# Kernel optimization log

Measured on AMD Instinct MI355X. Metric: run time of the kernel, lower is better.

The kernel has to match this reference:

```python
import jax, jax.numpy as jnp
import numpy as np

NEG_INF = -1.0e9  # matches the -1e9 mask constant in the torch module


def setup_inputs() -> dict:
    key = jax.random.key(0)
    k1, k2, k3, k4, k5 = jax.random.split(key, 5)
    B, S, D = 8, 2048, 1024
    x = jax.random.normal(k1, (B, S, D), dtype=jnp.float32)
    mask = jax.random.randint(k2, (B, S), 0, 2, dtype=jnp.int32)
    # torch.nn.Linear stores weight as [out_features, in_features]
    scale = 1.0 / np.sqrt(D)
    w_q = jax.random.normal(k3, (D, D), dtype=jnp.float32) * scale
    w_k = jax.random.normal(k4, (D, D), dtype=jnp.float32) * scale
    w_v = jax.random.normal(k5, (D, D), dtype=jnp.float32) * scale
    return {"x": x, "mask": mask, "w_q": w_q, "w_k": w_k, "w_v": w_v}


def reference(x, mask, w_q, w_k, w_v):
    # Linear (no bias): y = x @ W^T
    q = jnp.einsum("bsd,ed->bse", x, w_q)
    k = jnp.einsum("bsd,ed->bse", x, w_k)
    v = jnp.einsum("bsd,ed->bse", x, w_v)
    # raw (unscaled) scores, exactly as in the torch module
    s = jnp.einsum("bqd,bkd->bqk", q, k)  # [B, S, S]
    # dropout p=0.0 -> identity (eval mode); mask added AFTER dropout
    s = s + NEG_INF * mask.astype(s.dtype)[:, None, :]  # broadcast over query dim
    s = jax.nn.softmax(s, axis=-1)
    out = jnp.einsum("bqk,bkd->bqd", s, v)
    return out, s
```

## Files before the change

### kernel.cpp

```cpp
#include <hip/hip_runtime.h>

#define NEG_INF_F (-1.0e9f)

typedef _Float16 f16x8 __attribute__((ext_vector_type(8)));
typedef float f32x4 __attribute__((ext_vector_type(4)));

__device__ inline unsigned short f16_of(float f) {
    _Float16 h = (_Float16)f;
    return __builtin_bit_cast(unsigned short, h);
}
__device__ inline float f32_of(unsigned short u) {
    return (float)__builtin_bit_cast(_Float16, u);
}

__device__ inline void gload16(const unsigned short* g, unsigned short* l) {
    __builtin_amdgcn_global_load_lds(
        (const __attribute__((address_space(1))) unsigned int*)g,
        (__attribute__((address_space(3))) unsigned int*)l, 16, 0, 0);
}

__device__ inline f16x8 frag32(const unsigned short* t, int r, int ch) {
    return *reinterpret_cast<const f16x8*>(&t[r * 32 + (ch ^ ((r >> 1) & 3)) * 8]);
}
__device__ inline f16x8 frag64(const unsigned short* t, int r, int ch) {
    return *reinterpret_cast<const f16x8*>(&t[r * 64 + (ch ^ (r & 7)) * 8]);
}

__device__ inline void stage_256x32(const unsigned short* __restrict__ g0, int ldg, int k0,
                                    unsigned short* qbuf, int w, int lane) {
#pragma unroll
    for (int c = 0; c < 2; ++c) {
        const int r = c * 128 + w * 16 + (lane >> 2);
        const int co = ((lane & 3) ^ ((r >> 1) & 3)) * 8;
        gload16(g0 + (long long)r * ldg + k0 + co, qbuf + (c * 128 + w * 16) * 32);
    }
}
__device__ inline void stage_128x32(const unsigned short* __restrict__ g0, int ldg, int k0,
                                    unsigned short* qbuf, int w, int lane) {
    const int r = w * 16 + (lane >> 2);
    const int co = ((lane & 3) ^ ((r >> 1) & 3)) * 8;
    gload16(g0 + (long long)r * ldg + k0 + co, qbuf + (w * 16) * 32);
}

__global__ __launch_bounds__(512, 2) void gemm2(
    const unsigned short* __restrict__ Ah_g, const unsigned short* __restrict__ Al_g,
    int lda,
    const unsigned short* __restrict__ Bh_g, int ldb,
    unsigned short* __restrict__ Ch, int ldc, int K)
{
    constexpr int BUF = 16384;
    const int tid = threadIdx.x;
    const int w = tid >> 6, lane = tid & 63;
    const int wr = w & 1, wc = w >> 1;
    const int lr = lane & 15, lg = lane >> 4;
    const int rowBase = blockIdx.x * 128;
    const int colBase = blockIdx.y * 256;

    __shared__ unsigned short smem[32768];

    const unsigned short* Ah0 = Ah_g + (long long)rowBase * lda;
    const unsigned short* Al0 = Al_g + (long long)rowBase * lda;
    const unsigned short* Bh0 = Bh_g + (long long)colBase * ldb;

    f32x4 acc[4][4] = {};
    const int NT = K / 32;

    stage_128x32(Ah0, lda, 0, smem, w, lane);
    stage_128x32(Al0, lda, 0, smem + 4096, w, lane);
    stage_256x32(Bh0, ldb, 0, smem + 8192, w, lane);
    __syncthreads();

    for (int kt = 0; kt < NT; ++kt) {
        const unsigned short* cbuf = smem + (kt & 1) * BUF;
        if (kt + 1 < NT) {
            unsigned short* nbuf = smem + ((kt + 1) & 1) * BUF;
            const int k1 = (kt + 1) * 32;
            stage_128x32(Ah0, lda, k1, nbuf, w, lane);
            stage_128x32(Al0, lda, k1, nbuf + 4096, w, lane);
            stage_256x32(Bh0, ldb, k1, nbuf + 8192, w, lane);
        }
        const unsigned short* tAh = cbuf;
        const unsigned short* tAl = cbuf + 4096;
        const unsigned short* tB  = cbuf + 8192;
        f16x8 ah[4], al[4], bh[4];
#pragma unroll
        for (int i = 0; i < 4; ++i) {
            const int r = wr * 64 + i * 16 + lr;
            ah[i] = frag32(tAh, r, lg);
            al[i] = frag32(tAl, r, lg);
        }
#pragma unroll
        for (int j = 0; j < 4; ++j)
            bh[j] = frag32(tB, wc * 64 + j * 16 + lr, lg);
#pragma unroll
        for (int i = 0; i < 4; ++i)
#pragma unroll
            for (int j = 0; j < 4; ++j) {
                f32x4 a = acc[i][j];
                a = __builtin_amdgcn_mfma_f32_16x16x32_f16(ah[i], bh[j], a, 0, 0, 0);
                a = __builtin_amdgcn_mfma_f32_16x16x32_f16(al[i], bh[j], a, 0, 0, 0);
                acc[i][j] = a;
            }
        __syncthreads();
    }

    __syncthreads();
    float* stg = reinterpret_cast<float*>(smem) + w * 2048;
    const int colg0 = colBase + wc * 64;
#pragma unroll
    for (int rnd = 0; rnd < 2; ++rnd) {
        const int rowg0 = rowBase + wr * 64 + rnd * 32;
#pragma unroll
        for (int ii = 0; ii < 2; ++ii)
#pragma unroll
            for (int j = 0; j < 4; ++j)
#pragma unroll
                for (int r2 = 0; r2 < 4; ++r2)
                    stg[(ii * 16 + lg * 4 + r2) * 64 + j * 16 + lr] = acc[rnd * 2 + ii][j][r2];

#pragma unroll
        for (int t = 0; t < 8; ++t) {
            const int idx = t * 256 + lane * 4;
            const int r = idx >> 6, c = idx & 63;
            const float4 v = *reinterpret_cast<const float4*>(&stg[idx]);
            ushort4 h;
            h.x = f16_of(v.x); h.y = f16_of(v.y);
            h.z = f16_of(v.z); h.w = f16_of(v.w);
            *reinterpret_cast<ushort4*>(
                &Ch[(long long)(rowg0 + r) * ldc + colg0 + c]) = h;
        }
    }
}

__device__ inline void stage_ktile1(
    const unsigned short* __restrict__ Ah0, int lda,
    const unsigned short* __restrict__ Bh0, int ldb,
    int k0, unsigned short* buf, int w, int lane)
{
#pragma unroll
    for (int c = 0; c < 4; ++c) {
        const int r = c * 64 + w * 8 + (lane >> 3);
        const int co = ((lane & 7) ^ (r & 7)) * 8;
        const int lb = (c * 64 + w * 8) * 64;
        gload16(Ah0 + (long long)r * lda + k0 + co, buf + lb);
        gload16(Bh0 + (long long)r * ldb + k0 + co, buf + 16384 + lb);
    }
}

template <int OMODE>
__global__ __launch_bounds__(512, 2) void mfma_gemm1(
    const unsigned short* __restrict__ Ah_g, long long strideA, int lda,
    const unsigned short* __restrict__ Bh_g, long long strideB, int ldb,
    float* __restrict__ Cf, unsigned short* __restrict__ Ch, unsigned short* __restrict__ Ch2,
    long long strideC, int ldc, int K,
    const int* __restrict__ mask, long long strideMask)
{
    const int b = blockIdx.z;
    const int tid = threadIdx.x;
    const int w = tid >> 6, lane = tid & 63;
    const int wr = w >> 2, wc = w & 3;
    const int lr = lane & 15, lg = lane >> 4;
    const int rowBase = blockIdx.x * 256;
    const int colBase = blockIdx.y * 256;

    __shared__ unsigned short smem[65536];

    const unsigned short* Ah0 = Ah_g + (long long)b * strideA + (long long)rowBase * lda;
    const unsigned short* Bh0 = Bh_g + (long long)b * strideB + (long long)colBase * ldb;

    f32x4 acc[8][4] = {};
    const int NT = K / 64;

    stage_ktile1(Ah0, lda, Bh0, ldb, 0, smem, w, lane);
    __syncthreads();

    for (int kt = 0; kt < NT; ++kt) {
        const unsigned short* cbuf = smem + (kt & 1) * 32768;
        if (kt + 1 < NT)
            stage_ktile1(Ah0, lda, Bh0, ldb, (kt + 1) * 64,
                         smem + ((kt + 1) & 1) * 32768, w, lane);

        const unsigned short* tA = cbuf;
        const unsigned short* tB = cbuf + 16384;
        f16x8 bh[8];
#pragma unroll
        for (int j = 0; j < 4; ++j)
#pragma unroll
            for (int ks = 0; ks < 2; ++ks)
                bh[j * 2 + ks] = frag64(tB, wc * 64 + j * 16 + lr, ks * 4 + lg);
#pragma unroll
        for (int ih = 0; ih < 2; ++ih) {
            f16x8 ah[8];
#pragma unroll
            for (int f = 0; f < 4; ++f)
#pragma unroll
                for (int ks = 0; ks < 2; ++ks)
                    ah[f * 2 + ks] = frag64(tA, wr * 128 + ih * 64 + f * 16 + lr, ks * 4 + lg);
#pragma unroll
            for (int f = 0; f < 4; ++f)
#pragma unroll
                for (int j = 0; j < 4; ++j) {
                    f32x4 a = acc[ih * 4 + f][j];
                    a = __builtin_amdgcn_mfma_f32_16x16x32_f16(ah[f * 2 + 0], bh[j * 2 + 0], a, 0, 0, 0);
                    a = __builtin_amdgcn_mfma_f32_16x16x32_f16(ah[f * 2 + 1], bh[j * 2 + 1], a, 0, 0, 0);
                    acc[ih * 4 + f][j] = a;
                }
        }
        __syncthreads();
    }

    __syncthreads();
    float* stg = reinterpret_cast<float*>(smem) + w * 2048;
    const int colg0 = colBase + wc * 64;
#pragma unroll
    for (int rnd = 0; rnd < 4; ++rnd) {
        const int rowg0 = rowBase + wr * 128 + rnd * 32;
#pragma unroll
        for (int ii = 0; ii < 2; ++ii)
#pragma unroll
            for (int j = 0; j < 4; ++j)
#pragma unroll
                for (int r2 = 0; r2 < 4; ++r2)
                    stg[(ii * 16 + lg * 4 + r2) * 64 + j * 16 + lr] = acc[rnd * 2 + ii][j][r2];

        if constexpr (OMODE == 0) {
#pragma unroll
            for (int t = 0; t < 8; ++t) {
                const int idx = t * 256 + lane * 4;
                const int r = idx >> 6, c = idx & 63;
                float4 v = *reinterpret_cast<const float4*>(&stg[idx]);
                const int colg = colg0 + c;
                if (mask != nullptr) {
                    const int4 mv = *reinterpret_cast<const int4*>(
                        &mask[(long long)b * strideMask + colg]);
                    v.x += NEG_INF_F * (float)mv.x;
                    v.y += NEG_INF_F * (float)mv.y;
                    v.z += NEG_INF_F * (float)mv.z;
                    v.w += NEG_INF_F * (float)mv.w;
                }
                *reinterpret_cast<float4*>(
                    &Cf[(long long)b * strideC + (long long)(rowg0 + r) * ldc + colg]) = v;
            }
        } else {
            if (colBase < 1024) {
#pragma unroll
                for (int t = 0; t < 8; ++t) {
                    const int idx = t * 256 + lane * 4;
                    const int r = idx >> 6, c = idx & 63;
                    const float4 v = *reinterpret_cast<const float4*>(&stg[idx]);
                    ushort4 h;
                    h.x = f16_of(v.x); h.y = f16_of(v.y);
                    h.z = f16_of(v.z); h.w = f16_of(v.w);
                    *reinterpret_cast<ushort4*>(
                        &Ch[(long long)(rowg0 + r) * ldc + colg0 + c]) = h;
                }
            } else {
                const int b2 = rowg0 >> 11;
                const int s0 = rowg0 & 2047;
                const int vcol = colg0 - 1024 + lane;
                alignas(16) unsigned short u[32];
#pragma unroll
                for (int rr = 0; rr < 32; ++rr) u[rr] = f16_of(stg[rr * 64 + lane]);
                unsigned short* vp = Ch2 + (long long)b2 * (1024LL * 2048)
                                   + (long long)vcol * 2048 + s0;
#pragma unroll
                for (int q = 0; q < 4; ++q)
                    *reinterpret_cast<uint4*>(vp + q * 8) =
                        *reinterpret_cast<const uint4*>(&u[q * 8]);
            }
        }
        __syncthreads();
    }
}

__global__ __launch_bounds__(256) void cvt_kernel(
    const float* __restrict__ in, unsigned short* __restrict__ out, long long n)
{
    for (long long i = ((long long)blockIdx.x * 256 + threadIdx.x) * 4; i < n;
         i += (long long)gridDim.x * 256 * 4) {
        float4 v = *reinterpret_cast<const float4*>(&in[i]);
        ushort4 h;
        h.x = f16_of(v.x); h.y = f16_of(v.y); h.z = f16_of(v.z); h.w = f16_of(v.w);
        *reinterpret_cast<ushort4*>(&out[i]) = h;
    }
}

__global__ __launch_bounds__(256) void tsplit_kernel(
    const float* __restrict__ in, unsigned short* __restrict__ hi,
    unsigned short* __restrict__ lo, int N)
{
    __shared__ float tile[64][65];
    const int bi = blockIdx.x * 64;
    const int bj = blockIdx.y * 64;
    const int t = threadIdx.x;
    const int c4 = (t & 15) * 4;
    const int r0 = (t >> 4) * 4;
#pragma unroll
    for (int rr = 0; rr < 4; ++rr) {
        float4 v = *reinterpret_cast<const float4*>(
            &in[(long long)(bi + r0 + rr) * N + bj + c4]);
        tile[r0 + rr][c4 + 0] = v.x;
        tile[r0 + rr][c4 + 1] = v.y;
        tile[r0 + rr][c4 + 2] = v.z;
        tile[r0 + rr][c4 + 3] = v.w;
    }
    __syncthreads();
    const int oc  = t >> 2;
    const int or0 = (t & 3) * 16;
    alignas(16) unsigned short uh[16], ul[16];
#pragma unroll
    for (int e = 0; e < 16; ++e) {
        const float f = tile[or0 + e][oc];
        const unsigned short h = f16_of(f);
        uh[e] = h;
        ul[e] = f16_of(f - f32_of(h));
    }
    unsigned short* hp = hi + (long long)(bj + oc) * N + bi + or0;
    unsigned short* lp = lo + (long long)(bj + oc) * N + bi + or0;
    *reinterpret_cast<uint4*>(hp)     = *reinterpret_cast<const uint4*>(&uh[0]);
    *reinterpret_cast<uint4*>(hp + 8) = *reinterpret_cast<const uint4*>(&uh[8]);
    *reinterpret_cast<uint4*>(lp)     = *reinterpret_cast<const uint4*>(&ul[0]);
    *reinterpret_cast<uint4*>(lp + 8) = *reinterpret_cast<const uint4*>(&ul[8]);
}

__global__ __launch_bounds__(256) void softmax_kernel(
    float* __restrict__ s, unsigned short* __restrict__ p)
{
    const long long row = blockIdx.x;
    float* sp = s + row * 2048;
    const int tid = threadIdx.x;

    float v[8];
    *reinterpret_cast<float4*>(&v[0]) = *reinterpret_cast<const float4*>(&sp[tid * 8]);
    *reinterpret_cast<float4*>(&v[4]) = *reinterpret_cast<const float4*>(&sp[tid * 8 + 4]);

    float m = v[0];
#pragma unroll
    for (int i = 1; i < 8; ++i) m = fmaxf(m, v[i]);
#pragma unroll
    for (int off = 1; off < 64; off <<= 1) m = fmaxf(m, __shfl_xor(m, off));

    __shared__ float redm[4];
    __shared__ float reds[4];
    if ((tid & 63) == 0) redm[tid >> 6] = m;
    __syncthreads();
    m = fmaxf(fmaxf(redm[0], redm[1]), fmaxf(redm[2], redm[3]));

    float sum = 0.f;
#pragma unroll
    for (int i = 0; i < 8; ++i) {
        v[i] = __expf(v[i] - m);
        sum += v[i];
    }
#pragma unroll
    for (int off = 1; off < 64; off <<= 1) sum += __shfl_xor(sum, off);
    if ((tid & 63) == 0) reds[tid >> 6] = sum;
    __syncthreads();
    sum = reds[0] + reds[1] + reds[2] + reds[3];

    const float inv = 1.0f / sum;
#pragma unroll
    for (int i = 0; i < 8; ++i) v[i] *= inv;

    *reinterpret_cast<float4*>(&sp[tid * 8])     = *reinterpret_cast<const float4*>(&v[0]);
    *reinterpret_cast<float4*>(&sp[tid * 8 + 4]) = *reinterpret_cast<const float4*>(&v[4]);

    ushort4 o0, o1;
    o0.x = f16_of(v[0]); o0.y = f16_of(v[1]); o0.z = f16_of(v[2]); o0.w = f16_of(v[3]);
    o1.x = f16_of(v[4]); o1.y = f16_of(v[5]); o1.z = f16_of(v[6]); o1.w = f16_of(v[7]);
    *reinterpret_cast<ushort4*>(&p[row * 2048 + tid * 8])     = o0;
    *reinterpret_cast<ushort4*>(&p[row * 2048 + tid * 8 + 4]) = o1;
}

extern "C" void kernel_launch(void* const* d_in, const int* in_sizes, int n_in,
                              void* d_out, int out_size, void* d_ws, size_t ws_size,
                              hipStream_t stream)
{
    (void)in_sizes; (void)n_in; (void)out_size; (void)ws_size;

    const int S = 2048, D = 1024;
    const long long BS  = 8LL * S;
    const long long SD  = (long long)S * D;
    const long long SS  = (long long)S * S;
    const long long BSD = BS * D;
    const long long DD  = (long long)D * D;

    const float* x    = (const float*)d_in[0];
    const int*   mask = (const int*)d_in[1];
    const float* wq   = (const float*)d_in[2];
    const float* wk   = (const float*)d_in[3];
    const float* wv   = (const float*)d_in[4];

    float* out = (float*)d_out;
    float* s   = out + BSD;

    unsigned short* G    = (unsigned short*)d_ws;
    unsigned short* p    = G;
    unsigned short* Vt   = G + 2 * BSD;
    unsigned short* MtWv = G + 3 * BSD;
    unsigned short* Mth  = MtWv;
    unsigned short* wvh  = MtWv + DD;

    unsigned short* xh = (unsigned short*)out;
    unsigned short* wqTh = (unsigned short*)s;
    unsigned short* wqTl = wqTh + DD;
    unsigned short* wkTh = wqTl + DD;
    unsigned short* wkTl = wkTh + DD;

    dim3 blk256(256), blk512(512);

    cvt_kernel<<<dim3(4096), blk256, 0, stream>>>(x, xh, BSD);
    tsplit_kernel<<<dim3(16, 16), blk256, 0, stream>>>(wq, wqTh, wqTl, D);
    tsplit_kernel<<<dim3(16, 16), blk256, 0, stream>>>(wk, wkTh, wkTl, D);
    cvt_kernel<<<dim3(512), blk256, 0, stream>>>(wv, wvh, DD);

    gemm2<<<dim3(8, 4, 1), blk512, 0, stream>>>(
        wkTh, wkTl, D, wqTh, D, Mth, D, D);

    mfma_gemm1<4><<<dim3(64, 8, 1), blk512, 0, stream>>>(
        xh, 0, D, MtWv, 0, D,
        nullptr, G, Vt, 0, D, D, nullptr, 0);

    mfma_gemm1<0><<<dim3(8, 8, 8), blk512, 0, stream>>>(
        G, SD, D, xh, SD, D,
        s, nullptr, nullptr, SS, S, D, mask, S);

    softmax_kernel<<<dim3(16384), blk256, 0, stream>>>(s, p);

    mfma_gemm1<0><<<dim3(8, 4, 8), blk512, 0, stream>>>(
        p, SS, S, Vt, SD, S, out, nullptr, nullptr, SD, D, S, nullptr, 0);
}
```

Before: 322.3 us.

## Switch main GEMM to 32x32x16 MFMA and fuse weight prep kernels

The main tiled GEMM now uses 32x32x16 f16 MFMA instructions with 16-float accumulators instead of 16x16x32. This halves the number of MFMA issues and LDS fragment loads per k-tile, and the epilogue staging is remapped to the new accumulator layout. The three small weight preparation launches (two transpose-splits and one convert) are merged into one kernel indexed by blockIdx.z, which saves launch overhead. The risk is different register pressure and LDS bank behaviour with the new fragment pattern.

Result: slower. 333.8 us (+3.6%).

```diff
diff --git a/kernel.cpp b/kernel.cpp
--- a/kernel.cpp
+++ b/kernel.cpp
@@ -4,6 +4,7 @@
 
 typedef _Float16 f16x8 __attribute__((ext_vector_type(8)));
 typedef float f32x4 __attribute__((ext_vector_type(4)));
+typedef float f32x16 __attribute__((ext_vector_type(16)));
 
 __device__ inline unsigned short f16_of(float f) {
     _Float16 h = (_Float16)f;
@@ -159,7 +160,7 @@
     const int tid = threadIdx.x;
     const int w = tid >> 6, lane = tid & 63;
     const int wr = w >> 2, wc = w & 3;
-    const int lr = lane & 15, lg = lane >> 4;
+    const int ln31 = lane & 31, lhi = lane >> 5;
     const int rowBase = blockIdx.x * 256;
     const int colBase = blockIdx.y * 256;
 
@@ -168,7 +169,7 @@
     const unsigned short* Ah0 = Ah_g + (long long)b * strideA + (long long)rowBase * lda;
     const unsigned short* Bh0 = Bh_g + (long long)b * strideB + (long long)colBase * ldb;
 
-    f32x4 acc[8][4] = {};
+    f32x16 acc[4][2] = {};
     const int NT = K / 64;
 
     stage_ktile1(Ah0, lda, Bh0, ldb, 0, smem, w, lane);
@@ -182,29 +183,20 @@
 
         const unsigned short* tA = cbuf;
         const unsigned short* tB = cbuf + 16384;
-        f16x8 bh[8];
-#pragma unroll
-        for (int j = 0; j < 4; ++j)
-#pragma unroll
-            for (int ks = 0; ks < 2; ++ks)
-                bh[j * 2 + ks] = frag64(tB, wc * 64 + j * 16 + lr, ks * 4 + lg);
-#pragma unroll
-        for (int ih = 0; ih < 2; ++ih) {
-            f16x8 ah[8];
-#pragma unroll
-            for (int f = 0; f < 4; ++f)
-#pragma unroll
-                for (int ks = 0; ks < 2; ++ks)
-                    ah[f * 2 + ks] = frag64(tA, wr * 128 + ih * 64 + f * 16 + lr, ks * 4 + lg);
-#pragma unroll
-            for (int f = 0; f < 4; ++f)
-#pragma unroll
-                for (int j = 0; j < 4; ++j) {
-                    f32x4 a = acc[ih * 4 + f][j];
-                    a = __builtin_amdgcn_mfma_f32_16x16x32_f16(ah[f * 2 + 0], bh[j * 2 + 0], a, 0, 0, 0);
-                    a = __builtin_amdgcn_mfma_f32_16x16x32_f16(ah[f * 2 + 1], bh[j * 2 + 1], a, 0, 0, 0);
-                    acc[ih * 4 + f][j] = a;
-                }
+#pragma unroll
+        for (int ks = 0; ks < 4; ++ks) {
+            f16x8 bfr[2];
+#pragma unroll
+            for (int j = 0; j < 2; ++j)
+                bfr[j] = frag64(tB, wc * 64 + j * 32 + ln31, ks * 2 + lhi);
+#pragma unroll
+            for (int fi = 0; fi < 4; ++fi) {
+                const f16x8 afr = frag64(tA, wr * 128 + fi * 32 + ln31, ks * 2 + lhi);
+#pragma unroll
+                for (int j = 0; j < 2; ++j)
+                    acc[fi][j] = __builtin_amdgcn_mfma_f32_32x32x16_f16(
+                        afr, bfr[j], acc[fi][j], 0, 0, 0);
+            }
         }
         __syncthreads();
     }
@@ -216,12 +208,12 @@
     for (int rnd = 0; rnd < 4; ++rnd) {
         const int rowg0 = rowBase + wr * 128 + rnd * 32;
 #pragma unroll
-        for (int ii = 0; ii < 2; ++ii)
-#pragma unroll
-            for (int j = 0; j < 4; ++j)
-#pragma unroll
-                for (int r2 = 0; r2 < 4; ++r2)
-                    stg[(ii * 16 + lg * 4 + r2) * 64 + j * 16 + lr] = acc[rnd * 2 + ii][j][r2];
+        for (int fj = 0; fj < 2; ++fj)
+#pragma unroll
+            for (int reg = 0; reg < 16; ++reg) {
+                const int rif = (reg & 3) + 8 * (reg >> 2) + 4 * lhi;
+                stg[rif * 64 + fj * 32 + ln31] = acc[rnd][fj][reg];
+            }
 
         if constexpr (OMODE == 0) {
 #pragma unroll
@@ -285,14 +277,38 @@
     }
 }
 
-__global__ __launch_bounds__(256) void tsplit_kernel(
-    const float* __restrict__ in, unsigned short* __restrict__ hi,
-    unsigned short* __restrict__ lo, int N)
-{
-    __shared__ float tile[64][65];
+__global__ __launch_bounds__(256) void wprep_kernel(
+    const float* __restrict__ wq, const float* __restrict__ wk,
+    const float* __restrict__ wv,
+    unsigned short* __restrict__ wqTh, unsigned short* __restrict__ wqTl,
+    unsigned short* __restrict__ wkTh, unsigned short* __restrict__ wkTl,
+    unsigned short* __restrict__ wvh, int N)
+{
+    const int z = blockIdx.z;
     const int bi = blockIdx.x * 64;
     const int bj = blockIdx.y * 64;
     const int t = threadIdx.x;
+
+    if (z == 2) {
+        const int r = t >> 4;
+        const int c4 = (t & 15) * 4;
+#pragma unroll
+        for (int rr = 0; rr < 4; ++rr) {
+            const int row = bi + rr * 16 + r;
+            float4 v = *reinterpret_cast<const float4*>(&wv[(long long)row * N + bj + c4]);
+            ushort4 h;
+            h.x = f16_of(v.x); h.y = f16_of(v.y);
+            h.z = f16_of(v.z); h.w = f16_of(v.w);
+            *reinterpret_cast<ushort4*>(&wvh[(long long)row * N + bj + c4]) = h;
+        }
+        return;
+    }
+
+    const float* in = (z == 0) ? wq : wk;
+    unsigned short* hi = (z == 0) ? wqTh : wkTh;
+    unsigned short* lo = (z == 0) ? wqTl : wkTl;
+
+    __shared__ float tile[64][65];
     const int c4 = (t & 15) * 4;
     const int r0 = (t >> 4) * 4;
 #pragma unroll
@@ -410,9 +426,8 @@
     dim3 blk256(256), blk512(512);
 
     cvt_kernel<<<dim3(4096), blk256, 0, stream>>>(x, xh, BSD);
-    tsplit_kernel<<<dim3(16, 16), blk256, 0, stream>>>(wq, wqTh, wqTl, D);
-    tsplit_kernel<<<dim3(16, 16), blk256, 0, stream>>>(wk, wkTh, wkTl, D);
-    cvt_kernel<<<dim3(512), blk256, 0, stream>>>(wv, wvh, DD);
+    wprep_kernel<<<dim3(16, 16, 3), blk256, 0, stream>>>(
+        wq, wk, wv, wqTh, wqTl, wkTh, wkTl, wvh, D);
 
     gemm2<<<dim3(8, 4, 1), blk512, 0, stream>>>(
         wkTh, wkTl, D, wqTh, D, Mth, D, D);
```
